# Kernel tuning notes

Measured on AMD Instinct MI355X. Metric: run time of the kernel, lower is better.

The kernel has to match this reference:

```python
import jax, jax.numpy as jnp
import numpy as np

B, IN_F, OUT_F = 1024, 256, 256
GRID_SIZE, K = 5, 3  # grid_size, spline_order
N_BASIS = GRID_SIZE + K


def _make_grid():
    h = (1.0 - (-1.0)) / GRID_SIZE
    return jnp.linspace(-1.0 - K * h, 1.0 + K * h, GRID_SIZE + 2 * K + 1, dtype=jnp.float32)


def compute_bspline_basis(x, grid, k):
    # x: (N,), grid: (G + 2k + 1,) -> (N, G + k)
    x = x[:, None]
    bases = ((x >= grid[:-1]) & (x < grid[1:])).astype(x.dtype)
    for p in range(1, k + 1):
        n = bases.shape[1] - 1
        left_den = jnp.clip(grid[p:p + n] - grid[:n], 1e-8)
        left = (x - grid[:n]) / left_den * bases[:, :n]
        right_den = jnp.clip(grid[p + 1:p + 1 + n] - grid[1:1 + n], 1e-8)
        right = (grid[p + 1:p + 1 + n] - x) / right_den * bases[:, 1:1 + n]
        bases = left + right
    # boundary fix: x at/above last interior knot falls into last basis
    bases = bases.at[:, -1].add((x[:, 0] >= grid[-k - 1]).astype(x.dtype))
    return bases


def setup_inputs() -> dict:
    key = jax.random.key(0)
    kx, kc, kb = jax.random.split(key, 3)
    x = jax.random.normal(kx, (B, IN_F), dtype=jnp.float32)
    coeff = jax.random.normal(kc, (OUT_F, IN_F, N_BASIS), dtype=jnp.float32) / np.sqrt(IN_F * N_BASIS)
    base_weight = jax.random.normal(kb, (OUT_F, IN_F), dtype=jnp.float32) / np.sqrt(IN_F)
    spline_weight = jnp.ones((OUT_F, IN_F), dtype=jnp.float32)
    grid = _make_grid()
    return {"x": x, "grid": grid, "coeff": coeff,
            "base_weight": base_weight, "spline_weight": spline_weight}


def reference(x, grid, coeff, base_weight, spline_weight):
    batch = x.shape[0]
    bases = compute_bspline_basis(x.reshape(-1), grid, K)          # (B*in, n_basis)
    bases = bases.reshape(batch, IN_F, N_BASIS)                     # (b, i, n)
    spline_out = jnp.einsum('bin,oin->boi', bases, coeff)           # (b, o, i)
    spline_out = spline_out * spline_weight[None, :, :]
    base_out = jax.nn.silu(x)[:, None, :] * base_weight[None, :, :]  # (b, o, i)
    return (spline_out + base_out).sum(axis=2)                      # (b, o)
```

## Files before the change

kernel.cpp:

```cpp
#include <hip/hip_runtime.h>
#include <hip/hip_bf16.h>

#define B_SZ   1024
#define IN_F   256
#define OUT_F  256
#define NB     9
#define KTOT   (IN_F * NB)
#define NGRID  12

typedef __attribute__((ext_vector_type(8))) short  bf16x8;
typedef __attribute__((ext_vector_type(16))) float f32x16;

__global__ __launch_bounds__(256) void kan_prep(
    const float* __restrict__ x,
    const float* __restrict__ grid,
    const float* __restrict__ coeff,
    const float* __restrict__ bw,
    const float* __restrict__ sw,
    __hip_bfloat16* __restrict__ phi,
    __hip_bfloat16* __restrict__ W) {
  if (blockIdx.x < (B_SZ * IN_F) / 256) {
    int idx = blockIdx.x * 256 + threadIdx.x;
    float g[NGRID];
#pragma unroll
    for (int j = 0; j < NGRID; ++j) g[j] = grid[j];
    float xv = x[idx];

    float bas[NGRID - 1];
#pragma unroll
    for (int j = 0; j < NGRID - 1; ++j)
      bas[j] = (xv >= g[j] && xv < g[j + 1]) ? 1.0f : 0.0f;

#pragma unroll
    for (int p = 1; p <= 3; ++p) {
      int n = NGRID - 1 - p;
#pragma unroll
      for (int j = 0; j < n; ++j) {
        float ld = g[p + j] - g[j];
        if (ld < 1e-8f) ld = 1e-8f;
        float rd = g[p + 1 + j] - g[j + 1];
        if (rd < 1e-8f) rd = 1e-8f;
        bas[j] = (xv - g[j]) * __builtin_amdgcn_rcpf(ld) * bas[j] +
                 (g[p + 1 + j] - xv) * __builtin_amdgcn_rcpf(rd) * bas[j + 1];
      }
    }
    bas[7] += (xv >= g[NGRID - 4]) ? 1.0f : 0.0f;
    float sil = xv / (1.0f + __expf(-xv));

    int b = idx >> 8;
    int i = idx & 255;
    __hip_bfloat16* dst = phi + b * KTOT + i;
#pragma unroll
    for (int n = 0; n < 8; ++n) dst[n * IN_F] = __float2bfloat16(bas[n]);
    dst[8 * IN_F] = __float2bfloat16(sil);
  } else {
    int idx = (blockIdx.x - (B_SZ * IN_F) / 256) * 256 + threadIdx.x;
    int o = idx >> 8;
    int i = idx & 255;
    float s = sw[idx];
    const float* c = coeff + (size_t)idx * 8;
    __hip_bfloat16* dst = W + o * KTOT + i;
#pragma unroll
    for (int n = 0; n < 8; ++n)
      dst[n * IN_F] = __float2bfloat16(s * c[n]);
    dst[8 * IN_F] = __float2bfloat16(bw[idx]);
  }
}

#define KSEG (KTOT / 8)

__global__ __launch_bounds__(512) void kan_gemm(
    const __hip_bfloat16* __restrict__ phi,
    const __hip_bfloat16* __restrict__ W,
    float* __restrict__ out) {
  __shared__ float partial[8][32 * 32];

  int tid  = threadIdx.x;
  int wave = tid >> 6;
  int lane = tid & 63;
  int bm = (blockIdx.x & 31) * 32;
  int bn = (blockIdx.x >> 5) * 32;
  int r = lane & 31;
  int h = lane >> 5;

  const short* ap = (const short*)(phi + (size_t)(bm + r) * KTOT) + wave * KSEG + h * 8;
  const short* bp = (const short*)(W   + (size_t)(bn + r) * KTOT) + wave * KSEG + h * 8;

  f32x16 acc;
#pragma unroll
  for (int g = 0; g < 16; ++g) acc[g] = 0.0f;

#pragma unroll 6
  for (int k = 0; k < KSEG; k += 16) {
    bf16x8 a = *(const bf16x8*)(ap + k);
    bf16x8 b = *(const bf16x8*)(bp + k);
    acc = __builtin_amdgcn_mfma_f32_32x32x16_bf16(a, b, acc, 0, 0, 0);
  }

  float* pw = &partial[wave][0];
#pragma unroll
  for (int g = 0; g < 16; ++g) {
    int row = (g & 3) + 8 * (g >> 2) + 4 * h;
    pw[row * 32 + r] = acc[g];
  }
  __syncthreads();

  int e0 = tid * 2;
  float s0 = 0.0f, s1 = 0.0f;
#pragma unroll
  for (int w = 0; w < 8; ++w) {
    s0 += partial[w][e0];
    s1 += partial[w][e0 + 1];
  }
  int row = e0 >> 5, col = e0 & 31;
  float2 v = make_float2(s0, s1);
  *(float2*)&out[(size_t)(bm + row) * OUT_F + bn + col] = v;
}

extern "C" void kernel_launch(void* const* d_in, const int* in_sizes, int n_in,
                              void* d_out, int out_size, void* d_ws, size_t ws_size,
                              hipStream_t stream) {
  const float* x     = (const float*)d_in[0];
  const float* grid  = (const float*)d_in[1];
  const float* coeff = (const float*)d_in[2];
  const float* bw    = (const float*)d_in[3];
  const float* sw    = (const float*)d_in[4];
  float* out = (float*)d_out;

  __hip_bfloat16* phi = (__hip_bfloat16*)d_ws;
  __hip_bfloat16* W   = phi + (size_t)B_SZ * KTOT;

  kan_prep<<<(B_SZ * IN_F + OUT_F * IN_F) / 256, 256, 0, stream>>>(
      x, grid, coeff, bw, sw, phi, W);
  kan_gemm<<<(B_SZ / 32) * (OUT_F / 32), 512, 0, stream>>>(phi, W, out);
}
```

Measured before the change: 76.65 us.

## Double split-K waves in KAN GEMM and simplify uniform-grid spline recursion

The GEMM kernel now splits the K dimension across 16 waves per block instead of 8, using a two-phase shared-memory reduction, to raise per-CU parallelism given only 256 blocks. The prep kernel replaces per-knot reciprocal denominators with a single spacing-based reciprocal, assuming a uniform grid, and loads coefficients as float4. The uniform-grid assumption ties correctness to the linspace grid, and the extra reduction phase adds a barrier.

New measurement: 75.35 us. No clear change (-1.7%).

```diff
diff --git a/kernel.cpp b/kernel.cpp
--- a/kernel.cpp
+++ b/kernel.cpp
@@ -31,17 +31,17 @@
     for (int j = 0; j < NGRID - 1; ++j)
       bas[j] = (xv >= g[j] && xv < g[j + 1]) ? 1.0f : 0.0f;
 
+    float h = g[1] - g[0];
+    float r1 = __builtin_amdgcn_rcpf(h);
+    float rp[3] = { r1, 0.5f * r1, (1.0f / 3.0f) * r1 };
+
 #pragma unroll
     for (int p = 1; p <= 3; ++p) {
       int n = NGRID - 1 - p;
+      float inv = rp[p - 1];
 #pragma unroll
       for (int j = 0; j < n; ++j) {
-        float ld = g[p + j] - g[j];
-        if (ld < 1e-8f) ld = 1e-8f;
-        float rd = g[p + 1 + j] - g[j + 1];
-        if (rd < 1e-8f) rd = 1e-8f;
-        bas[j] = (xv - g[j]) * __builtin_amdgcn_rcpf(ld) * bas[j] +
-                 (g[p + 1 + j] - xv) * __builtin_amdgcn_rcpf(rd) * bas[j + 1];
+        bas[j] = ((xv - g[j]) * bas[j] + (g[p + 1 + j] - xv) * bas[j + 1]) * inv;
       }
     }
     bas[7] += (xv >= g[NGRID - 4]) ? 1.0f : 0.0f;
@@ -49,7 +49,7 @@
 
     int b = idx >> 8;
     int i = idx & 255;
-    __hip_bfloat16* dst = phi + b * KTOT + i;
+    __hip_bfloat16* dst = phi + (size_t)b * KTOT + i;
 #pragma unroll
     for (int n = 0; n < 8; ++n) dst[n * IN_F] = __float2bfloat16(bas[n]);
     dst[8 * IN_F] = __float2bfloat16(sil);
@@ -58,18 +58,25 @@
     int o = idx >> 8;
     int i = idx & 255;
     float s = sw[idx];
-    const float* c = coeff + (size_t)idx * 8;
-    __hip_bfloat16* dst = W + o * KTOT + i;
-#pragma unroll
-    for (int n = 0; n < 8; ++n)
-      dst[n * IN_F] = __float2bfloat16(s * c[n]);
+    const float4* c4 = (const float4*)(coeff + (size_t)idx * 8);
+    float4 c0 = c4[0];
+    float4 c1 = c4[1];
+    __hip_bfloat16* dst = W + (size_t)o * KTOT + i;
+    dst[0 * IN_F] = __float2bfloat16(s * c0.x);
+    dst[1 * IN_F] = __float2bfloat16(s * c0.y);
+    dst[2 * IN_F] = __float2bfloat16(s * c0.z);
+    dst[3 * IN_F] = __float2bfloat16(s * c0.w);
+    dst[4 * IN_F] = __float2bfloat16(s * c1.x);
+    dst[5 * IN_F] = __float2bfloat16(s * c1.y);
+    dst[6 * IN_F] = __float2bfloat16(s * c1.z);
+    dst[7 * IN_F] = __float2bfloat16(s * c1.w);
     dst[8 * IN_F] = __float2bfloat16(bw[idx]);
   }
 }
 
-#define KSEG (KTOT / 8)
+#define KSEG (KTOT / 16)
 
-__global__ __launch_bounds__(512) void kan_gemm(
+__global__ __launch_bounds__(1024) void kan_gemm(
     const __hip_bfloat16* __restrict__ phi,
     const __hip_bfloat16* __restrict__ W,
     float* __restrict__ out) {
@@ -90,31 +97,36 @@
 #pragma unroll
   for (int g = 0; g < 16; ++g) acc[g] = 0.0f;
 
-#pragma unroll 6
+#pragma unroll 3
   for (int k = 0; k < KSEG; k += 16) {
     bf16x8 a = *(const bf16x8*)(ap + k);
     bf16x8 b = *(const bf16x8*)(bp + k);
     acc = __builtin_amdgcn_mfma_f32_32x32x16_bf16(a, b, acc, 0, 0, 0);
   }
 
-  float* pw = &partial[wave][0];
+  float* pw = &partial[wave & 7][0];
+  if (wave < 8) {
 #pragma unroll
-  for (int g = 0; g < 16; ++g) {
-    int row = (g & 3) + 8 * (g >> 2) + 4 * h;
-    pw[row * 32 + r] = acc[g];
+    for (int g = 0; g < 16; ++g) {
+      int row = (g & 3) + 8 * (g >> 2) + 4 * h;
+      pw[row * 32 + r] = acc[g];
+    }
+  }
+  __syncthreads();
+  if (wave >= 8) {
+#pragma unroll
+    for (int g = 0; g < 16; ++g) {
+      int row = (g & 3) + 8 * (g >> 2) + 4 * h;
+      pw[row * 32 + r] += acc[g];
+    }
   }
   __syncthreads();
 
-  int e0 = tid * 2;
-  float s0 = 0.0f, s1 = 0.0f;
+  float s = 0.0f;
 #pragma unroll
-  for (int w = 0; w < 8; ++w) {
-    s0 += partial[w][e0];
-    s1 += partial[w][e0 + 1];
-  }
-  int row = e0 >> 5, col = e0 & 31;
-  float2 v = make_float2(s0, s1);
-  *(float2*)&out[(size_t)(bm + row) * OUT_F + bn + col] = v;
+  for (int w = 0; w < 8; ++w) s += partial[w][tid];
+  int row = tid >> 5, col = tid & 31;
+  out[(size_t)(bm + row) * OUT_F + bn + col] = s;
 }
 
 extern "C" void kernel_launch(void* const* d_in, const int* in_sizes, int n_in,
@@ -132,5 +144,5 @@
 
   kan_prep<<<(B_SZ * IN_F + OUT_F * IN_F) / 256, 256, 0, stream>>>(
       x, grid, coeff, bw, sw, phi, W);
-  kan_gemm<<<(B_SZ / 32) * (OUT_F / 32), 512, 0, stream>>>(phi, W, out);
+  kan_gemm<<<(B_SZ / 32) * (OUT_F / 32), 1024, 0, stream>>>(phi, W, out);
 }
```
